# Optimization experiments

Measured on AMD Instinct MI355X. Metric: run time of the kernel, lower is better.

## Reference

```python
import jax, jax.numpy as jnp
import numpy as np
from jax import lax

P = 4
PSIZE = P * P
ITERS = 3
EPS = 1e-8
LAMBDA = 1e-3  # inverse-temperature used by the EM routing sigmoid (yl-1993 style)
LN2PI_HALF = 0.5 * float(np.log(2.0 * np.pi))


def extract_patches(x, K, stride, pad):
    """x: (b,h,w,c) -> (b,oh,ow,K*K,c) sliding-window patches."""
    if pad:
        x = jnp.pad(x, ((0, 0), (pad, pad), (pad, pad), (0, 0)))
    b, h, w, c = x.shape
    oh = (h - K) // stride + 1
    ow = (w - K) // stride + 1
    slices = []
    for ki in range(K):
        for kj in range(K):
            slices.append(x[:, ki:ki + stride * (oh - 1) + 1:stride,
                             kj:kj + stride * (ow - 1) + 1:stride, :])
    return jnp.stack(slices, axis=3)  # (b,oh,ow,K*K,c)


def em_routing(v, a_in, beta_u, beta_a, iters=ITERS):
    """EM routing (Hinton et al. 2018).
    v: (n, Bin, Cout, PSIZE) votes, a_in: (n, Bin, 1) input activations.
    Returns mu: (n, Cout, PSIZE), a_out: (n, Cout).
    """
    n, Bin, Cout, psize = v.shape
    r = jnp.full((n, Bin, Cout), 1.0 / Cout, dtype=v.dtype)
    mu = None
    a_out = None
    for it in range(iters):
        # ---- M step ----
        r_w = r * a_in                                    # (n,Bin,Cout)
        r_sum = r_w.sum(axis=1, keepdims=True)            # (n,1,Cout)
        coeff = (r_w / (r_sum + EPS))[..., None]          # (n,Bin,Cout,1)
        mu = jnp.sum(coeff * v, axis=1, keepdims=True)    # (n,1,Cout,psize)
        sigma_sq = jnp.sum(coeff * (v - mu) ** 2, axis=1, keepdims=True) + EPS
        cost_h = (beta_u[None, None, :, None] + 0.5 * jnp.log(sigma_sq)) * r_sum[..., None]
        a_out = jax.nn.sigmoid(LAMBDA * (beta_a[None, None, :] - cost_h.sum(axis=3)))  # (n,1,Cout)
        # ---- E step ----
        if it < iters - 1:
            ln_p = -(v - mu) ** 2 / (2.0 * sigma_sq) - 0.5 * jnp.log(sigma_sq) - LN2PI_HALF
            ln_ap = ln_p.sum(axis=3) + jnp.log(EPS + a_out)  # (n,Bin,Cout)
            r = jax.nn.softmax(ln_ap, axis=2)
    return mu[:, 0], a_out[:, 0]


def depthwise_caps(pose, a, W, bu, ba, K, stride):
    """DepthWiseConvCaps: each capsule type routes its own KxK spatial patch to one
    output capsule of the same type. W: (K*K, B, P, P)."""
    b = pose.shape[0]
    Bc = a.shape[-1]
    pad = K // 2
    pp = extract_patches(pose, K, stride, pad)  # (b,oh,ow,KK,B*PSIZE)
    ap = extract_patches(a, K, stride, pad)     # (b,oh,ow,KK,B)
    oh, ow = pp.shape[1], pp.shape[2]
    pm = pp.reshape(b, oh, ow, K * K, Bc, P, P)
    v = jnp.einsum('bhwkcij,kcjl->bhwkcil', pm, W)            # (b,oh,ow,KK,B,P,P)
    v = v.transpose(0, 1, 2, 4, 3, 5, 6).reshape(b * oh * ow * Bc, K * K, 1, PSIZE)
    a_in = ap.transpose(0, 1, 2, 4, 3).reshape(b * oh * ow * Bc, K * K, 1)
    mu, a_out = em_routing(v, a_in, bu, ba)
    return mu.reshape(b, oh, ow, Bc * PSIZE), a_out.reshape(b, oh, ow, Bc)


def conv_caps_1x1(pose, a, W, bu, ba):
    """ConvCaps with K=1, stride=1: per-position routing Bin -> Cout. W: (Bin,Cout,P,P)."""
    b, h, w, _ = pose.shape
    Bc, Cc = W.shape[0], W.shape[1]
    pm = pose.reshape(b * h * w, Bc, P, P)
    v = jnp.einsum('nbij,bcjl->nbcil', pm, W).reshape(b * h * w, Bc, Cc, PSIZE)
    a_in = a.reshape(b * h * w, Bc)[..., None]
    mu, a_out = em_routing(v, a_in, bu, ba)
    return mu.reshape(b, h, w, Cc * PSIZE), a_out.reshape(b, h, w, Cc)


def class_caps(pose, a, W, bu, ba):
    """Class ConvCaps: w_shared across positions + coordinate addition. W: (D,E,P,P)."""
    b, h, w, _ = pose.shape
    D, E = W.shape[0], W.shape[1]
    pm = pose.reshape(b, h, w, D, P, P)
    v = jnp.einsum('bhwdij,dejl->bhwdeil', pm, W).reshape(b, h, w, D, E, PSIZE)
    # coordinate addition on the first two vote components
    coord = jnp.zeros((h, w, PSIZE), v.dtype)
    coord = coord.at[:, :, 0].add(jnp.arange(h, dtype=v.dtype)[:, None] / h)
    coord = coord.at[:, :, 1].add(jnp.arange(w, dtype=v.dtype)[None, :] / w)
    v = v + coord[None, :, :, None, None, :]
    v = v.reshape(b, h * w * D, E, PSIZE)
    a_in = a.reshape(b, h * w * D, 1)
    mu, a_out = em_routing(v, a_in, bu, ba)
    return mu, a_out  # (b,E,PSIZE), (b,E)


def _forward(x, conv1_w, conv1_b, prim_pose_w, prim_pose_b, prim_a_w, prim_a_b,
             dw1_w, dw1_bu, dw1_ba, cc1_w, cc1_bu, cc1_ba,
             dw2_w, dw2_bu, dw2_ba, cc2_w, cc2_bu, cc2_ba,
             cls_w, cls_bu, cls_ba):
    # conv stem: k5 s2 valid
    y = lax.conv_general_dilated(x, conv1_w, (2, 2), 'VALID',
                                 dimension_numbers=('NHWC', 'HWIO', 'NHWC'))
    y = jax.nn.relu(y + conv1_b)
    # primary caps: 1x1 convs for pose and activation
    pose = jnp.einsum('bhwc,cd->bhwd', y, prim_pose_w) + prim_pose_b   # (b,h,w,B*PSIZE)
    a = jax.nn.sigmoid(jnp.einsum('bhwc,cd->bhwd', y, prim_a_w) + prim_a_b)  # (b,h,w,B)
    pose, a = depthwise_caps(pose, a, dw1_w, dw1_bu, dw1_ba, K=7, stride=2)
    pose, a = conv_caps_1x1(pose, a, cc1_w, cc1_bu, cc1_ba)
    pose, a = depthwise_caps(pose, a, dw2_w, dw2_bu, dw2_ba, K=5, stride=2)
    pose, a = conv_caps_1x1(pose, a, cc2_w, cc2_bu, cc2_ba)
    pose_cls, a_cls = class_caps(pose, a, cls_w, cls_bu, cls_ba)
    return a_cls  # (b, E)


def setup_inputs() -> dict:
    key = jax.random.key(0)
    ks = jax.random.split(key, 10)
    f32 = jnp.float32
    d = {}
    d['x'] = jax.random.normal(ks[0], (32, 64, 64, 1), f32)
    d['conv1_w'] = jax.random.normal(ks[1], (5, 5, 1, 64), f32) * 0.1
    d['conv1_b'] = jnp.zeros((64,), f32)
    d['prim_pose_w'] = jax.random.normal(ks[2], (64, 128), f32) * 0.1
    d['prim_pose_b'] = jnp.zeros((128,), f32)
    d['prim_a_w'] = jax.random.normal(ks[3], (64, 8), f32) * 0.1
    d['prim_a_b'] = jnp.zeros((8,), f32)
    d['dw1_w'] = jax.random.normal(ks[4], (49, 8, 4, 4), f32) * 0.25
    d['dw1_bu'] = jnp.zeros((1,), f32)
    d['dw1_ba'] = jnp.zeros((1,), f32)
    d['cc1_w'] = jax.random.normal(ks[5], (8, 16, 4, 4), f32) * 0.25
    d['cc1_bu'] = jnp.zeros((16,), f32)
    d['cc1_ba'] = jnp.zeros((16,), f32)
    d['dw2_w'] = jax.random.normal(ks[6], (25, 16, 4, 4), f32) * 0.25
    d['dw2_bu'] = jnp.zeros((1,), f32)
    d['dw2_ba'] = jnp.zeros((1,), f32)
    d['cc2_w'] = jax.random.normal(ks[7], (16, 16, 4, 4), f32) * 0.25
    d['cc2_bu'] = jnp.zeros((16,), f32)
    d['cc2_ba'] = jnp.zeros((16,), f32)
    d['cls_w'] = jax.random.normal(ks[8], (16, 10, 4, 4), f32) * 0.25
    d['cls_bu'] = jnp.zeros((10,), f32)
    d['cls_ba'] = jnp.zeros((10,), f32)
    return d


def reference(x, conv1_w, conv1_b, prim_pose_w, prim_pose_b, prim_a_w, prim_a_b,
              dw1_w, dw1_bu, dw1_ba, cc1_w, cc1_bu, cc1_ba,
              dw2_w, dw2_bu, dw2_ba, cc2_w, cc2_bu, cc2_ba,
              cls_w, cls_bu, cls_ba):
    return _forward(x, conv1_w, conv1_b, prim_pose_w, prim_pose_b, prim_a_w, prim_a_b,
                    dw1_w, dw1_bu, dw1_ba, cc1_w, cc1_bu, cc1_ba,
                    dw2_w, dw2_bu, dw2_ba, cc2_w, cc2_bu, cc2_ba,
                    cls_w, cls_bu, cls_ba)
```

## Files before the change

### kernel.cpp

```cpp
#include <hip/hip_runtime.h>
#include <hip/hip_bf16.h>

#define EPS 1e-8f
#define LAMBDA 1e-3f
#define LN2PI_HALF 0.9189385332046727f

__device__ __forceinline__ float sigmoidf(float x) { return 1.f / (1.f + __expf(-x)); }

__global__ __launch_bounds__(256) void stem_primary_kernel(
    const float* __restrict__ x, const float* __restrict__ w,
    const float* __restrict__ bias,
    const float* __restrict__ wp, const float* __restrict__ bp,
    const float* __restrict__ wa, const float* __restrict__ ba,
    float* __restrict__ pose, float* __restrict__ a) {
  __shared__ __align__(16) float wc_s[25][64];
  __shared__ __align__(16) float wa_s[64][8];
  __shared__ __align__(16) float bias_s[64];
  __shared__ __align__(16) float bp_s[128];
  __shared__ float ba_s[8];
  __shared__ float xs[5][63];
  __shared__ __align__(16) float ys_u[2][15][68];

  int t = threadIdx.x;
  int oi = blockIdx.x % 30;
  int b  = blockIdx.x / 30;

  for (int q = t; q < 400;  q += 256) ((float4*)wc_s)[q] = ((const float4*)w)[q];
  for (int q = t; q < 128;  q += 256) ((float4*)wa_s)[q] = ((const float4*)wa)[q];
  if (t < 64) bias_s[t] = bias[t];
  if (t < 128) bp_s[t] = bp[t];
  if (t < 8) ba_s[t] = ba[t];
  for (int q = t; q < 315; q += 256) {
    int ki = q / 63, col = q % 63;
    xs[ki][col] = x[(b * 64 + 2 * oi + ki) * 64 + col];
  }
  __syncthreads();

  for (int q = t; q < 480; q += 256) {
    int pos = q >> 4, c4 = (q & 15) << 2;
    float4 s4 = *(const float4*)&bias_s[c4];
#pragma unroll
    for (int ki = 0; ki < 5; ++ki)
#pragma unroll
      for (int kj = 0; kj < 5; ++kj) {
        float xv = xs[ki][2 * pos + kj];
        const float4 wv = *(const float4*)&wc_s[ki * 5 + kj][c4];
        s4.x += xv * wv.x;
        s4.y += xv * wv.y;
        s4.z += xv * wv.z;
        s4.w += xv * wv.w;
      }
    s4.x = fmaxf(s4.x, 0.f);
    s4.y = fmaxf(s4.y, 0.f);
    s4.z = fmaxf(s4.z, 0.f);
    s4.w = fmaxf(s4.w, 0.f);
    *(float4*)&ys_u[pos & 1][pos >> 1][c4] = s4;
  }
  __syncthreads();

  int w_ = t >> 7, d = t & 127;
  float acc[15];
#pragma unroll
  for (int j = 0; j < 15; ++j) acc[j] = bp_s[d];
  const float* wpd = wp + d;
#pragma unroll 4
  for (int c4 = 0; c4 < 64; c4 += 4) {
    float w0 = wpd[(c4 + 0) * 128];
    float w1 = wpd[(c4 + 1) * 128];
    float w2 = wpd[(c4 + 2) * 128];
    float w3 = wpd[(c4 + 3) * 128];
#pragma unroll
    for (int j = 0; j < 15; ++j) {
      const float4 yv = *(const float4*)&ys_u[w_][j][c4];
      acc[j] += yv.x * w0 + yv.y * w1 + yv.z * w2 + yv.w * w3;
    }
  }
  size_t rowb = (size_t)(b * 30 + oi) * 30;
#pragma unroll
  for (int j = 0; j < 15; ++j)
    pose[(rowb + w_ + 2 * j) * 128 + d] = acc[j];

  if (t < 240) {
    int pos = t >> 3, jj = t & 7;
    float s = ba_s[jj];
#pragma unroll 8
    for (int c = 0; c < 64; ++c) s += ys_u[pos & 1][pos >> 1][c] * wa_s[c][jj];
    a[(rowb + pos) * 8 + jj] = sigmoidf(s);
  }
}

template <int K, int BC, int HIN, int WIN, int HOUT, int WOUT, int OIG, int NG>
__global__ __launch_bounds__(256) void dw_caps_kernel(
    const float* __restrict__ pose_in, const float* __restrict__ a_in,
    const float* __restrict__ Wt,
    const float* __restrict__ bu_p, const float* __restrict__ ba_p,
    float* __restrict__ pose_out, float* __restrict__ a_out) {
  constexpr int PAD = K / 2;
  constexpr int RA = (2 * (OIG - 1) + K < HIN) ? (2 * (OIG - 1) + K) : HIN;
  constexpr int TOT = OIG * WOUT * 16;
  constexpr int KM = (TOT + 255) / 256;
  __shared__ __align__(16) float tp[RA * WIN * 20];
  __shared__ float ta[RA * WIN];
  __shared__ __align__(16) float wt[K * K * 16];

  int t = threadIdx.x;
  int g = (NG > 1) ? (blockIdx.x % NG) : 0;
  int c = (blockIdx.x / NG) % BC;
  int b = blockIdx.x / (NG * BC);
  int oi_lo = g * OIG;
  int rlo = max(0, 2 * oi_lo - PAD);
  int rhi = min(HIN, 2 * (oi_lo + OIG - 1) - PAD + K);
  int nrows = rhi - rlo;

  for (int q = t; q < K * K * 16; q += 256) {
    int tap = q >> 4, lj = q & 15, l = lj >> 2, j = lj & 3;
    wt[tap * 16 + lj] = Wt[((size_t)tap * BC + c) * 16 + j * 4 + l];
  }
  for (int q = t; q < nrows * WIN; q += 256) {
    int row = q / WIN, col = q % WIN;
    ta[q] = a_in[((size_t)((b * HIN + rlo + row) * WIN + col)) * BC + c];
  }
  for (int q = t; q < nrows * WIN * 4; q += 256) {
    int quad = q & 3, pc = q >> 2;
    int row = pc / WIN, col = pc % WIN;
    const float4 src = *(const float4*)(pose_in +
        (((size_t)((b * HIN + rlo + row) * WIN + col)) * BC + c) * 16 + quad * 4);
    *(float4*)(tp + (row * WIN + col) * 20 + quad * 4) = src;
  }
  __syncthreads();

  const int p = t & 15;
  const int ip = p >> 2, l = p & 3;
  const float* wtl = wt + l * 4;

  int ih0[KM], iw0[KM];
  float rsum[KM], acc[KM], acc2[KM];
#pragma unroll
  for (int k = 0; k < KM; ++k) {
    int s = t + k * 256;
    int pr = s >> 4;
    int oj = pr % WOUT;
    int oi = oi_lo + pr / WOUT;
    ih0[k] = 2 * oi - PAD;
    iw0[k] = 2 * oj - PAD;
    rsum[k] = 0.f;
    acc[k] = 0.f;
    acc2[k] = 0.f;
  }

#pragma unroll 1
  for (int ki = 0; ki < K; ++ki) {
    int rb[KM];
    bool vk[KM];
#pragma unroll
    for (int k = 0; k < KM; ++k) {
      int ih = ih0[k] + ki;
      vk[k] = (t + k * 256 < TOT) && (ih >= 0) && (ih < HIN);
      rb[k] = (ih - rlo) * WIN;
    }
#pragma unroll
    for (int kj = 0; kj < K; ++kj) {
      const float4 wr = *(const float4*)(wtl + (ki * K + kj) * 16);
#pragma unroll
      for (int k = 0; k < KM; ++k) {
        if (!vk[k]) continue;
        int iw = iw0[k] + kj;
        if (iw < 0 || iw >= WIN) continue;
        int idx = rb[k] + iw;
        float ak = ta[idx];
        const float4 pm = *(const float4*)(tp + idx * 20 + ip * 4);
        float v = pm.x * wr.x + pm.y * wr.y + pm.z * wr.z + pm.w * wr.w;
        rsum[k] += ak;
        float av = ak * v;
        acc[k] += av;
        acc2[k] += av * v;
      }
    }
  }

#pragma unroll 1
  for (int k = 0; k < KM; ++k) {
    int s = t + k * 256;
    if (s >= TOT) break;
    int pr = s >> 4;
    int oj = pr % WOUT;
    int oi = oi_lo + pr / WOUT;
    float inv = 1.f / (rsum[k] + EPS);
    float mu = acc[k] * inv;
    float S = rsum[k] * inv;
    float sg = acc2[k] * inv - mu * mu * (2.f - S);
    sg = fmaxf(sg, 0.f) + EPS;
    float hl = 0.5f * __logf(sg);
    float ls = hl;
    ls += __shfl_xor(ls, 1, 64);
    ls += __shfl_xor(ls, 2, 64);
    ls += __shfl_xor(ls, 4, 64);
    ls += __shfl_xor(ls, 8, 64);

    size_t obase = ((size_t)(b * HOUT + oi) * WOUT + oj) * BC + c;
    pose_out[obase * 16 + p] = mu;
    if (p == 0) {
      float cost = rsum[k] * (16.f * bu_p[0] + ls);
      a_out[obase] = sigmoidf(LAMBDA * (ba_p[0] - cost));
    }
  }
}

__global__ __launch_bounds__(256) void cc_em_coop8_kernel(
    const float* __restrict__ pose_in, const float* __restrict__ a_arr,
    const float* __restrict__ Wt,
    const float* __restrict__ bu_p, const float* __restrict__ ba_p,
    float* __restrict__ pose_out, float* __restrict__ a_out) {
  __shared__ float red_s[2][2][2][64 * 9];
  int t = threadIdx.x;
  int w = t >> 6, lane = t & 63;
  int prob = w >> 1, wh = w & 1;
  int c = lane >> 2, q = lane & 3;
  int n = blockIdx.x * 2 + prob;

  float ain[4], rw[4], v[4][4];
  const float* pbase = pose_in + (size_t)n * 128;
#pragma unroll
  for (int i = 0; i < 4; ++i) {
    int b = wh * 4 + i;
    ain[i] = a_arr[(size_t)n * 8 + b];
    rw[i] = (1.f / 16.f) * ain[i];
    const float4 pm = *(const float4*)(pbase + b * 16 + q * 4);
    const float* wr = Wt + (b * 16 + c) * 16;
    const float4 r0 = *(const float4*)(wr + 0);
    const float4 r1 = *(const float4*)(wr + 4);
    const float4 r2 = *(const float4*)(wr + 8);
    const float4 r3 = *(const float4*)(wr + 12);
    v[i][0] = pm.x * r0.x + pm.y * r1.x + pm.z * r2.x + pm.w * r3.x;
    v[i][1] = pm.x * r0.y + pm.y * r1.y + pm.z * r2.y + pm.w * r3.y;
    v[i][2] = pm.x * r0.z + pm.y * r1.z + pm.z * r2.z + pm.w * r3.z;
    v[i][3] = pm.x * r0.w + pm.y * r1.w + pm.z * r2.w + pm.w * r3.w;
  }
  float bu = bu_p[c], ba = ba_p[c];

  float mu[4], inv2[4], lsum = 0.f, ao = 0.f;
#pragma unroll 1
  for (int it = 0; it < 3; ++it) {
    float psA = 0.f, psV[4] = {0, 0, 0, 0}, psV2[4] = {0, 0, 0, 0};
#pragma unroll
    for (int i = 0; i < 4; ++i) {
      psA += rw[i];
#pragma unroll
      for (int l = 0; l < 4; ++l) {
        float rv = rw[i] * v[i][l];
        psV[l] += rv;
        psV2[l] += rv * v[i][l];
      }
    }
    {
      float* rs = &red_s[it & 1][prob][wh][lane * 9];
      rs[0] = psA;
#pragma unroll
      for (int l = 0; l < 4; ++l) { rs[1 + l] = psV[l]; rs[5 + l] = psV2[l]; }
    }
    __syncthreads();
    float sA = 0.f, sV[4] = {0, 0, 0, 0}, sV2[4] = {0, 0, 0, 0};
#pragma unroll
    for (int w2 = 0; w2 < 2; ++w2) {
      const float* rr = &red_s[it & 1][prob][w2][lane * 9];
      sA += rr[0];
#pragma unroll
      for (int l = 0; l < 4; ++l) { sV[l] += rr[1 + l]; sV2[l] += rr[5 + l]; }
    }
    float inv = 1.f / (sA + EPS);
    float S = sA * inv;
    lsum = 0.f;
#pragma unroll
    for (int l = 0; l < 4; ++l) {
      mu[l] = sV[l] * inv;
      float sg = sV2[l] * inv - mu[l] * mu[l] * (2.f - S) + EPS;
      sg = fmaxf(sg, EPS);
      inv2[l] = 0.5f / sg;
      lsum += 0.5f * __logf(sg);
    }
    lsum += __shfl_xor(lsum, 1, 64);
    lsum += __shfl_xor(lsum, 2, 64);
    float cost = sA * (16.f * bu + lsum);
    ao = sigmoidf(LAMBDA * (ba - cost));

    if (it < 2) {
      float term[4];
#pragma unroll
      for (int i = 0; i < 4; ++i) {
        float s = 0.f;
#pragma unroll
        for (int l = 0; l < 4; ++l) {
          float d = v[i][l] - mu[l];
          s += d * d * inv2[l];
        }
        term[i] = s;
      }
#pragma unroll
      for (int i = 0; i < 4; ++i) {
        term[i] += __shfl_xor(term[i], 1, 64);
        term[i] += __shfl_xor(term[i], 2, 64);
      }
      float basec = __logf(EPS + ao) - lsum - 16.f * LN2PI_HALF;
      float lnap[4], mx[4], Z[4];
#pragma unroll
      for (int i = 0; i < 4; ++i) { lnap[i] = basec - term[i]; mx[i] = lnap[i]; }
#pragma unroll
      for (int m = 4; m < 64; m <<= 1)
#pragma unroll
        for (int i = 0; i < 4; ++i) mx[i] = fmaxf(mx[i], __shfl_xor(mx[i], m, 64));
#pragma unroll
      for (int i = 0; i < 4; ++i) { lnap[i] = __expf(lnap[i] - mx[i]); Z[i] = lnap[i]; }
#pragma unroll
      for (int m = 4; m < 64; m <<= 1)
#pragma unroll
        for (int i = 0; i < 4; ++i) Z[i] += __shfl_xor(Z[i], m, 64);
#pragma unroll
      for (int i = 0; i < 4; ++i) rw[i] = lnap[i] / Z[i] * ain[i];
    }
  }
  if (wh == 0) {
    *(float4*)(pose_out + (size_t)n * 256 + c * 16 + q * 4) =
        make_float4(mu[0], mu[1], mu[2], mu[3]);
    if (q == 0) a_out[(size_t)n * 16 + c] = ao;
  }
}

__global__ __launch_bounds__(256) void cc_em_coop16_kernel(
    const float* __restrict__ pose_in, const float* __restrict__ a_arr,
    const float* __restrict__ Wt,
    const float* __restrict__ bu_p, const float* __restrict__ ba_p,
    float* __restrict__ pose_out, float* __restrict__ a_out) {
  __shared__ float red_s[2][4][64 * 9];
  int t = threadIdx.x;
  int w = t >> 6, lane = t & 63;
  int c = lane >> 2, q = lane & 3;
  int n = blockIdx.x;

  float ain[4], rw[4], v[4][4];
  const float* pbase = pose_in + (size_t)n * 256;
#pragma unroll
  for (int i = 0; i < 4; ++i) {
    int b = w * 4 + i;
    ain[i] = a_arr[(size_t)n * 16 + b];
    rw[i] = (1.f / 16.f) * ain[i];
    const float4 pm = *(const float4*)(pbase + b * 16 + q * 4);
    const float* wr = Wt + (b * 16 + c) * 16;
    const float4 r0 = *(const float4*)(wr + 0);
    const float4 r1 = *(const float4*)(wr + 4);
    const float4 r2 = *(const float4*)(wr + 8);
    const float4 r3 = *(const float4*)(wr + 12);
    v[i][0] = pm.x * r0.x + pm.y * r1.x + pm.z * r2.x + pm.w * r3.x;
    v[i][1] = pm.x * r0.y + pm.y * r1.y + pm.z * r2.y + pm.w * r3.y;
    v[i][2] = pm.x * r0.z + pm.y * r1.z + pm.z * r2.z + pm.w * r3.z;
    v[i][3] = pm.x * r0.w + pm.y * r1.w + pm.z * r2.w + pm.w * r3.w;
  }
  float bu = bu_p[c], ba = ba_p[c];

  float mu[4], inv2[4], lsum = 0.f, ao = 0.f;
#pragma unroll 1
  for (int it = 0; it < 3; ++it) {
    float psA = 0.f, psV[4] = {0, 0, 0, 0}, psV2[4] = {0, 0, 0, 0};
#pragma unroll
    for (int i = 0; i < 4; ++i) {
      psA += rw[i];
#pragma unroll
      for (int l = 0; l < 4; ++l) {
        float rv = rw[i] * v[i][l];
        psV[l] += rv;
        psV2[l] += rv * v[i][l];
      }
    }
    {
      float* rs = &red_s[it & 1][w][lane * 9];
      rs[0] = psA;
#pragma unroll
      for (int l = 0; l < 4; ++l) { rs[1 + l] = psV[l]; rs[5 + l] = psV2[l]; }
    }
    __syncthreads();
    float sA = 0.f, sV[4] = {0, 0, 0, 0}, sV2[4] = {0, 0, 0, 0};
#pragma unroll
    for (int w2 = 0; w2 < 4; ++w2) {
      const float* rr = &red_s[it & 1][w2][lane * 9];
      sA += rr[0];
#pragma unroll
      for (int l = 0; l < 4; ++l) { sV[l] += rr[1 + l]; sV2[l] += rr[5 + l]; }
    }
    float inv = 1.f / (sA + EPS);
    float S = sA * inv;
    lsum = 0.f;
#pragma unroll
    for (int l = 0; l < 4; ++l) {
      mu[l] = sV[l] * inv;
      float sg = sV2[l] * inv - mu[l] * mu[l] * (2.f - S) + EPS;
      sg = fmaxf(sg, EPS);
      inv2[l] = 0.5f / sg;
      lsum += 0.5f * __logf(sg);
    }
    lsum += __shfl_xor(lsum, 1, 64);
    lsum += __shfl_xor(lsum, 2, 64);
    float cost = sA * (16.f * bu + lsum);
    ao = sigmoidf(LAMBDA * (ba - cost));

    if (it < 2) {
      float term[4];
#pragma unroll
      for (int i = 0; i < 4; ++i) {
        float s = 0.f;
#pragma unroll
        for (int l = 0; l < 4; ++l) {
          float d = v[i][l] - mu[l];
          s += d * d * inv2[l];
        }
        term[i] = s;
      }
#pragma unroll
      for (int i = 0; i < 4; ++i) {
        term[i] += __shfl_xor(term[i], 1, 64);
        term[i] += __shfl_xor(term[i], 2, 64);
      }
      float basec = __logf(EPS + ao) - lsum - 16.f * LN2PI_HALF;
      float lnap[4], mx[4], Z[4];
#pragma unroll
      for (int i = 0; i < 4; ++i) { lnap[i] = basec - term[i]; mx[i] = lnap[i]; }
#pragma unroll
      for (int m = 4; m < 64; m <<= 1)
#pragma unroll
        for (int i = 0; i < 4; ++i) mx[i] = fmaxf(mx[i], __shfl_xor(mx[i], m, 64));
#pragma unroll
      for (int i = 0; i < 4; ++i) { lnap[i] = __expf(lnap[i] - mx[i]); Z[i] = lnap[i]; }
#pragma unroll
      for (int m = 4; m < 64; m <<= 1)
#pragma unroll
        for (int i = 0; i < 4; ++i) Z[i] += __shfl_xor(Z[i], m, 64);
#pragma unroll
      for (int i = 0; i < 4; ++i) rw[i] = lnap[i] / Z[i] * ain[i];
    }
  }
  if (w == 0) {
    *(float4*)(pose_out + (size_t)n * 256 + c * 16 + q * 4) =
        make_float4(mu[0], mu[1], mu[2], mu[3]);
    if (q == 0) a_out[(size_t)n * 16 + c] = ao;
  }
}

__global__ __launch_bounds__(256) void cls_m_kernel(
    const float* __restrict__ pose5, const float* __restrict__ a5,
    const float* __restrict__ X, const float* __restrict__ W,
    const float* __restrict__ bu_p, const float* __restrict__ ba_p,
    float* __restrict__ mu_g, float* __restrict__ inv2_g,
    float* __restrict__ base_g, float* __restrict__ out,
    int first, int last) {
  int blk = blockIdx.x;
  int c = blk % 10, b = blk / 10;
  int t = threadIdx.x;
  int lane = t & 63, wv = t >> 6;
  const float* pg = pose5 + (size_t)b * 16384;
  __shared__ float w_s[16][16];
  {
    int d = t & 15, jj = t >> 4;
    w_s[jj][d] = W[(d * 10 + c) * 16 + jj];
  }
  __syncthreads();
  const int d = t & 15;
  float wf[16];
#pragma unroll
  for (int jj = 0; jj < 16; ++jj) wf[jj] = w_s[jj][d];

  float sA = 0.f, sV[16], sV2[16];
#pragma unroll
  for (int p = 0; p < 16; ++p) { sV[p] = 0.f; sV2[p] = 0.f; }
#pragma unroll 1
  for (int rep = 0; rep < 4; ++rep) {
    int bi = rep * 256 + t;
    int pos = bi >> 4;
    float rw = first ? 0.1f * a5[(size_t)b * 1024 + bi]
                     : X[(size_t)blk * 1024 + bi];
    float ci = (float)(pos >> 3) * 0.125f;
    float cj = (float)(pos & 7) * 0.125f;
    const float* pp = pg + pos * 256 + d * 16;
    float pmr[16];
#pragma unroll
    for (int q = 0; q < 16; ++q) pmr[q] = pp[q];
    sA += rw;
#pragma unroll
    for (int p = 0; p < 16; ++p) {
      int ip = p >> 2, l = p & 3;
      float v = pmr[ip * 4 + 0] * wf[0 * 4 + l] + pmr[ip * 4 + 1] * wf[1 * 4 + l]
              + pmr[ip * 4 + 2] * wf[2 * 4 + l] + pmr[ip * 4 + 3] * wf[3 * 4 + l];
      if (p == 0) v += ci;
      else if (p == 1) v += cj;
      float rv = rw * v;
      sV[p] += rv;
      sV2[p] += rv * v;
    }
  }
#pragma unroll
  for (int off = 1; off < 64; off <<= 1) {
    sA += __shfl_xor(sA, off, 64);
#pragma unroll
    for (int p = 0; p < 16; ++p) {
      sV[p]  += __shfl_xor(sV[p],  off, 64);
      sV2[p] += __shfl_xor(sV2[p], off, 64);
    }
  }
  __shared__ float red[4][36];
  if (lane == 0) {
    red[wv][0] = sA;
#pragma unroll
    for (int p = 0; p < 16; ++p) { red[wv][1 + p] = sV[p]; red[wv][17 + p] = sV2[p]; }
  }
  __syncthreads();
  if (t < 16) {
    int p = t;
    float sAf  = red[0][0] + red[1][0] + red[2][0] + red[3][0];
    float sVf  = red[0][1+p] + red[1][1+p] + red[2][1+p] + red[3][1+p];
    float sV2f = red[0][17+p] + red[1][17+p] + red[2][17+p] + red[3][17+p];
    float inv = 1.f / (sAf + EPS);
    float S = sAf * inv;
    float mu = sVf * inv;
    float sg = sV2f * inv - mu * mu * (2.f - S) + EPS;
    sg = fmaxf(sg, EPS);
    mu_g[blk * 16 + p] = mu;
    inv2_g[blk * 16 + p] = 0.5f / sg;
    float hl = 0.5f * __logf(sg);
    float lsum = hl;
    lsum += __shfl_xor(lsum, 1, 64);
    lsum += __shfl_xor(lsum, 2, 64);
    lsum += __shfl_xor(lsum, 4, 64);
    lsum += __shfl_xor(lsum, 8, 64);
    if (p == 0) {
      float cost = sAf * (16.f * bu_p[c] + lsum);
      float ao = sigmoidf(LAMBDA * (ba_p[c] - cost));
      base_g[blk] = __logf(EPS + ao) - lsum - 16.f * LN2PI_HALF;
      if (last) out[blk] = ao;
    }
  }
}

__global__ __launch_bounds__(256) void cls_e_kernel(
    const float* __restrict__ pose5, const float* __restrict__ a5,
    const float* __restrict__ W,
    const float* __restrict__ mu_g, const float* __restrict__ inv2_g,
    const float* __restrict__ base_g, float* __restrict__ X) {
  int b = blockIdx.x >> 2;
  int t = threadIdx.x;
  int bi = ((blockIdx.x & 3) << 8) + t;
  const float* pg = pose5 + (size_t)b * 16384;
  __shared__ float w2[10][16][16];
  __shared__ float mu_s[160];
  __shared__ float inv2_s[160];
  __shared__ float base_s[10];
  for (int q = t; q < 2560; q += 256) {
    int dd = q & 15, jj = (q >> 4) & 15, c = q >> 8;
    w2[c][jj][dd] = W[(dd * 10 + c) * 16 + jj];
  }
  if (t < 160) { mu_s[t] = mu_g[b * 160 + t]; inv2_s[t] = inv2_g[b * 160 + t]; }
  if (t >= 160 && t < 170) base_s[t - 160] = base_g[b * 10 + (t - 160)];
  __syncthreads();

  int pos = bi >> 4, d2 = bi & 15;
  float ci = (float)(pos >> 3) * 0.125f;
  float cj = (float)(pos & 7) * 0.125f;
  const float* pp = pg + pos * 256 + d2 * 16;
  float pmr[16];
#pragma unroll
  for (int q = 0; q < 16; ++q) pmr[q] = pp[q];
  float lnap[10];
#pragma unroll 1
  for (int c = 0; c < 10; ++c) {
    float wf[16];
#pragma unroll
    for (int jj = 0; jj < 16; ++jj) wf[jj] = w2[c][jj][d2];
    float s = base_s[c];
#pragma unroll
    for (int p = 0; p < 16; ++p) {
      int ip = p >> 2, l = p & 3;
      float v = pmr[ip * 4 + 0] * wf[0 * 4 + l] + pmr[ip * 4 + 1] * wf[1 * 4 + l]
              + pmr[ip * 4 + 2] * wf[2 * 4 + l] + pmr[ip * 4 + 3] * wf[3 * 4 + l];
      if (p == 0) v += ci;
      else if (p == 1) v += cj;
      float dd = v - mu_s[c * 16 + p];
      s -= dd * dd * inv2_s[c * 16 + p];
    }
    lnap[c] = s;
  }
  float m = -1e30f;
#pragma unroll
  for (int c = 0; c < 10; ++c) m = fmaxf(m, lnap[c]);
  float Z = 0.f;
  float ex[10];
#pragma unroll
  for (int c = 0; c < 10; ++c) { ex[c] = __expf(lnap[c] - m); Z += ex[c]; }
  float invZ = a5[(size_t)b * 1024 + bi] / Z;
#pragma unroll
  for (int c = 0; c < 10; ++c) X[((size_t)(b * 10 + c)) * 1024 + bi] = ex[c] * invZ;
}

extern "C" void kernel_launch(void* const* d_in, const int* in_sizes, int n_in,
                              void* d_out, int out_size, void* d_ws, size_t ws_size,
                              hipStream_t stream) {
  const float* x       = (const float*)d_in[0];
  const float* conv1_w = (const float*)d_in[1];
  const float* conv1_b = (const float*)d_in[2];
  const float* pp_w    = (const float*)d_in[3];
  const float* pp_b    = (const float*)d_in[4];
  const float* pa_w    = (const float*)d_in[5];
  const float* pa_b    = (const float*)d_in[6];
  const float* dw1_w   = (const float*)d_in[7];
  const float* dw1_bu  = (const float*)d_in[8];
  const float* dw1_ba  = (const float*)d_in[9];
  const float* cc1_w   = (const float*)d_in[10];
  const float* cc1_bu  = (const float*)d_in[11];
  const float* cc1_ba  = (const float*)d_in[12];
  const float* dw2_w   = (const float*)d_in[13];
  const float* dw2_bu  = (const float*)d_in[14];
  const float* dw2_ba  = (const float*)d_in[15];
  const float* cc2_w   = (const float*)d_in[16];
  const float* cc2_bu  = (const float*)d_in[17];
  const float* cc2_ba  = (const float*)d_in[18];
  const float* cls_w   = (const float*)d_in[19];
  const float* cls_bu  = (const float*)d_in[20];
  const float* cls_ba  = (const float*)d_in[21];
  float* out = (float*)d_out;

  float* ws = (float*)d_ws;
  float* pose1 = ws;
  float* a1    = ws + 3686400;
  float* pose2 = ws + 3916800;
  float* a2    = ws + 4838400;
  float* pose3 = ws;
  float* a3    = ws + 1843200;
  float* pose4 = ws + 1958400;
  float* a4    = ws + 2482688;
  float* pose5 = ws + 2515456;
  float* a5    = ws + 3039744;
  float* Xbuf  = ws + 3072512;
  float* mu_g  = ws + 3400192;
  float* inv2_g= ws + 3405312;
  float* base_g= ws + 3410432;

  stem_primary_kernel<<<960, 256, 0, stream>>>(x, conv1_w, conv1_b,
                                               pp_w, pp_b, pa_w, pa_b, pose1, a1);
  dw_caps_kernel<7, 8, 30, 30, 15, 15, 3, 5><<<1280, 256, 0, stream>>>(
      pose1, a1, dw1_w, dw1_bu, dw1_ba, pose2, a2);
  cc_em_coop8_kernel<<<3600, 256, 0, stream>>>(pose2, a2, cc1_w, cc1_bu, cc1_ba,
                                               pose3, a3);
  dw_caps_kernel<5, 16, 15, 15, 8, 8, 2, 4><<<2048, 256, 0, stream>>>(
      pose3, a3, dw2_w, dw2_bu, dw2_ba, pose4, a4);
  cc_em_coop16_kernel<<<2048, 256, 0, stream>>>(pose4, a4, cc2_w, cc2_bu, cc2_ba,
                                                pose5, a5);
  cls_m_kernel<<<320, 256, 0, stream>>>(pose5, a5, Xbuf, cls_w, cls_bu, cls_ba,
                                        mu_g, inv2_g, base_g, out, 1, 0);
  cls_e_kernel<<<128, 256, 0, stream>>>(pose5, a5, cls_w, mu_g, inv2_g, base_g, Xbuf);
  cls_m_kernel<<<320, 256, 0, stream>>>(pose5, a5, Xbuf, cls_w, cls_bu, cls_ba,
                                        mu_g, inv2_g, base_g, out, 0, 0);
  cls_e_kernel<<<128, 256, 0, stream>>>(pose5, a5, cls_w, mu_g, inv2_g, base_g, Xbuf);
  cls_m_kernel<<<320, 256, 0, stream>>>(pose5, a5, Xbuf, cls_w, cls_bu, cls_ba,
                                        mu_g, inv2_g, base_g, out, 0, 1);
}
```

Baseline: 250.3 us.

## Fuse class-capsule E-step into M-step kernel with ping-pong routing buffers

Merges the class-layer E step into the following M step, so each (batch, class) block recomputes the softmax over all 10 classes for its own inputs instead of reading a precomputed responsibility buffer. This drops two launches and the global round-trip through the X buffer. In exchange every block redoes the vote and log-likelihood computation for all classes, roughly ten times the E-step arithmetic. Double-buffered mu/inv2/base arrays prevent read/write races between iterations.

```diff
diff --git a/kernel.cpp b/kernel.cpp
--- a/kernel.cpp
+++ b/kernel.cpp
@@ -445,11 +445,10 @@
 
 __global__ __launch_bounds__(256) void cls_m_kernel(
     const float* __restrict__ pose5, const float* __restrict__ a5,
-    const float* __restrict__ X, const float* __restrict__ W,
+    const float* __restrict__ W,
     const float* __restrict__ bu_p, const float* __restrict__ ba_p,
     float* __restrict__ mu_g, float* __restrict__ inv2_g,
-    float* __restrict__ base_g, float* __restrict__ out,
-    int first, int last) {
+    float* __restrict__ base_g) {
   int blk = blockIdx.x;
   int c = blk % 10, b = blk / 10;
   int t = threadIdx.x;
@@ -473,8 +472,7 @@
   for (int rep = 0; rep < 4; ++rep) {
     int bi = rep * 256 + t;
     int pos = bi >> 4;
-    float rw = first ? 0.1f * a5[(size_t)b * 1024 + bi]
-                     : X[(size_t)blk * 1024 + bi];
+    float rw = 0.1f * a5[(size_t)b * 1024 + bi];
     float ci = (float)(pos >> 3) * 0.125f;
     float cj = (float)(pos & 7) * 0.125f;
     const float* pp = pg + pos * 256 + d * 16;
@@ -532,68 +530,129 @@
       float cost = sAf * (16.f * bu_p[c] + lsum);
       float ao = sigmoidf(LAMBDA * (ba_p[c] - cost));
       base_g[blk] = __logf(EPS + ao) - lsum - 16.f * LN2PI_HALF;
-      if (last) out[blk] = ao;
     }
   }
 }
 
-__global__ __launch_bounds__(256) void cls_e_kernel(
+__global__ __launch_bounds__(256) void cls_em_kernel(
     const float* __restrict__ pose5, const float* __restrict__ a5,
     const float* __restrict__ W,
-    const float* __restrict__ mu_g, const float* __restrict__ inv2_g,
-    const float* __restrict__ base_g, float* __restrict__ X) {
-  int b = blockIdx.x >> 2;
+    const float* __restrict__ bu_p, const float* __restrict__ ba_p,
+    const float* __restrict__ mu_in, const float* __restrict__ inv2_in,
+    const float* __restrict__ base_in,
+    float* __restrict__ mu_o, float* __restrict__ inv2_o,
+    float* __restrict__ base_o, float* __restrict__ out, int last) {
+  int blk = blockIdx.x;
+  int c_m = blk % 10, b = blk / 10;
   int t = threadIdx.x;
-  int bi = ((blockIdx.x & 3) << 8) + t;
+  int lane = t & 63, wv = t >> 6;
   const float* pg = pose5 + (size_t)b * 16384;
+
   __shared__ float w2[10][16][16];
   __shared__ float mu_s[160];
   __shared__ float inv2_s[160];
   __shared__ float base_s[10];
+  __shared__ float red[4][36];
+
   for (int q = t; q < 2560; q += 256) {
     int dd = q & 15, jj = (q >> 4) & 15, c = q >> 8;
     w2[c][jj][dd] = W[(dd * 10 + c) * 16 + jj];
   }
-  if (t < 160) { mu_s[t] = mu_g[b * 160 + t]; inv2_s[t] = inv2_g[b * 160 + t]; }
-  if (t >= 160 && t < 170) base_s[t - 160] = base_g[b * 10 + (t - 160)];
+  if (t < 160) { mu_s[t] = mu_in[b * 160 + t]; inv2_s[t] = inv2_in[b * 160 + t]; }
+  if (t >= 160 && t < 170) base_s[t - 160] = base_in[b * 10 + (t - 160)];
   __syncthreads();
 
-  int pos = bi >> 4, d2 = bi & 15;
-  float ci = (float)(pos >> 3) * 0.125f;
-  float cj = (float)(pos & 7) * 0.125f;
-  const float* pp = pg + pos * 256 + d2 * 16;
-  float pmr[16];
-#pragma unroll
-  for (int q = 0; q < 16; ++q) pmr[q] = pp[q];
-  float lnap[10];
+  const int d = t & 15;
+  float sA = 0.f, sV[16], sV2[16];
+#pragma unroll
+  for (int p = 0; p < 16; ++p) { sV[p] = 0.f; sV2[p] = 0.f; }
+
 #pragma unroll 1
-  for (int c = 0; c < 10; ++c) {
-    float wf[16];
-#pragma unroll
-    for (int jj = 0; jj < 16; ++jj) wf[jj] = w2[c][jj][d2];
-    float s = base_s[c];
+  for (int rep = 0; rep < 4; ++rep) {
+    int bi = rep * 256 + t;
+    int pos = bi >> 4;
+    float ci = (float)(pos >> 3) * 0.125f;
+    float cj = (float)(pos & 7) * 0.125f;
+    const float* pp = pg + pos * 256 + d * 16;
+    float pmr[16];
+#pragma unroll
+    for (int q = 0; q < 16; ++q) pmr[q] = pp[q];
+    float ain = a5[(size_t)b * 1024 + bi];
+
+    float vc[16];
+    float m_r = -1e30f, Z_r = 0.f, lnap_cm = 0.f;
+#pragma unroll 1
+    for (int c = 0; c < 10; ++c) {
+      float wf[16];
+#pragma unroll
+      for (int jj = 0; jj < 16; ++jj) wf[jj] = w2[c][jj][d];
+      float s = base_s[c];
+#pragma unroll
+      for (int p = 0; p < 16; ++p) {
+        int ip = p >> 2, l = p & 3;
+        float v = pmr[ip * 4 + 0] * wf[0 * 4 + l] + pmr[ip * 4 + 1] * wf[1 * 4 + l]
+                + pmr[ip * 4 + 2] * wf[2 * 4 + l] + pmr[ip * 4 + 3] * wf[3 * 4 + l];
+        if (p == 0) v += ci;
+        else if (p == 1) v += cj;
+        if (c == c_m) vc[p] = v;
+        float dd2 = v - mu_s[c * 16 + p];
+        s -= dd2 * dd2 * inv2_s[c * 16 + p];
+      }
+      if (c == c_m) lnap_cm = s;
+      if (s > m_r) { Z_r = Z_r * __expf(m_r - s) + 1.f; m_r = s; }
+      else Z_r += __expf(s - m_r);
+    }
+    float rw = __expf(lnap_cm - m_r) / Z_r * ain;
+
+    sA += rw;
 #pragma unroll
     for (int p = 0; p < 16; ++p) {
-      int ip = p >> 2, l = p & 3;
-      float v = pmr[ip * 4 + 0] * wf[0 * 4 + l] + pmr[ip * 4 + 1] * wf[1 * 4 + l]
-              + pmr[ip * 4 + 2] * wf[2 * 4 + l] + pmr[ip * 4 + 3] * wf[3 * 4 + l];
-      if (p == 0) v += ci;
-      else if (p == 1) v += cj;
-      float dd = v - mu_s[c * 16 + p];
-      s -= dd * dd * inv2_s[c * 16 + p];
-    }
-    lnap[c] = s;
-  }
-  float m = -1e30f;
-#pragma unroll
-  for (int c = 0; c < 10; ++c) m = fmaxf(m, lnap[c]);
-  float Z = 0.f;
-  float ex[10];
-#pragma unroll
-  for (int c = 0; c < 10; ++c) { ex[c] = __expf(lnap[c] - m); Z += ex[c]; }
-  float invZ = a5[(size_t)b * 1024 + bi] / Z;
-#pragma unroll
-  for (int c = 0; c < 10; ++c) X[((size_t)(b * 10 + c)) * 1024 + bi] = ex[c] * invZ;
+      float rv = rw * vc[p];
+      sV[p] += rv;
+      sV2[p] += rv * vc[p];
+    }
+  }
+
+#pragma unroll
+  for (int off = 1; off < 64; off <<= 1) {
+    sA += __shfl_xor(sA, off, 64);
+#pragma unroll
+    for (int p = 0; p < 16; ++p) {
+      sV[p]  += __shfl_xor(sV[p],  off, 64);
+      sV2[p] += __shfl_xor(sV2[p], off, 64);
+    }
+  }
+  if (lane == 0) {
+    red[wv][0] = sA;
+#pragma unroll
+    for (int p = 0; p < 16; ++p) { red[wv][1 + p] = sV[p]; red[wv][17 + p] = sV2[p]; }
+  }
+  __syncthreads();
+  if (t < 16) {
+    int p = t;
+    float sAf  = red[0][0] + red[1][0] + red[2][0] + red[3][0];
+    float sVf  = red[0][1+p] + red[1][1+p] + red[2][1+p] + red[3][1+p];
+    float sV2f = red[0][17+p] + red[1][17+p] + red[2][17+p] + red[3][17+p];
+    float inv = 1.f / (sAf + EPS);
+    float S = sAf * inv;
+    float mu = sVf * inv;
+    float sg = sV2f * inv - mu * mu * (2.f - S) + EPS;
+    sg = fmaxf(sg, EPS);
+    mu_o[blk * 16 + p] = mu;
+    inv2_o[blk * 16 + p] = 0.5f / sg;
+    float hl = 0.5f * __logf(sg);
+    float lsum = hl;
+    lsum += __shfl_xor(lsum, 1, 64);
+    lsum += __shfl_xor(lsum, 2, 64);
+    lsum += __shfl_xor(lsum, 4, 64);
+    lsum += __shfl_xor(lsum, 8, 64);
+    if (p == 0) {
+      float cost = sAf * (16.f * bu_p[c_m] + lsum);
+      float ao = sigmoidf(LAMBDA * (ba_p[c_m] - cost));
+      base_o[blk] = __logf(EPS + ao) - lsum - 16.f * LN2PI_HALF;
+      if (last) out[blk] = ao;
+    }
+  }
 }
 
 extern "C" void kernel_launch(void* const* d_in, const int* in_sizes, int n_in,
@@ -634,10 +693,12 @@
   float* a4    = ws + 2482688;
   float* pose5 = ws + 2515456;
   float* a5    = ws + 3039744;
-  float* Xbuf  = ws + 3072512;
-  float* mu_g  = ws + 3400192;
-  float* inv2_g= ws + 3405312;
-  float* base_g= ws + 3410432;
+  float* mu_gA  = ws + 3072512;
+  float* inv2_gA= ws + 3077632;
+  float* base_gA= ws + 3082752;
+  float* mu_gB  = ws + 3083072;
+  float* inv2_gB= ws + 3088192;
+  float* base_gB= ws + 3093312;
 
   stem_primary_kernel<<<960, 256, 0, stream>>>(x, conv1_w, conv1_b,
                                                pp_w, pp_b, pa_w, pa_b, pose1, a1);
@@ -649,12 +710,12 @@
       pose3, a3, dw2_w, dw2_bu, dw2_ba, pose4, a4);
   cc_em_coop16_kernel<<<2048, 256, 0, stream>>>(pose4, a4, cc2_w, cc2_bu, cc2_ba,
                                                 pose5, a5);
-  cls_m_kernel<<<320, 256, 0, stream>>>(pose5, a5, Xbuf, cls_w, cls_bu, cls_ba,
-                                        mu_g, inv2_g, base_g, out, 1, 0);
-  cls_e_kernel<<<128, 256, 0, stream>>>(pose5, a5, cls_w, mu_g, inv2_g, base_g, Xbuf);
-  cls_m_kernel<<<320, 256, 0, stream>>>(pose5, a5, Xbuf, cls_w, cls_bu, cls_ba,
-                                        mu_g, inv2_g, base_g, out, 0, 0);
-  cls_e_kernel<<<128, 256, 0, stream>>>(pose5, a5, cls_w, mu_g, inv2_g, base_g, Xbuf);
-  cls_m_kernel<<<320, 256, 0, stream>>>(pose5, a5, Xbuf, cls_w, cls_bu, cls_ba,
-                                        mu_g, inv2_g, base_g, out, 0, 1);
+  cls_m_kernel<<<320, 256, 0, stream>>>(pose5, a5, cls_w, cls_bu, cls_ba,
+                                        mu_gA, inv2_gA, base_gA);
+  cls_em_kernel<<<320, 256, 0, stream>>>(pose5, a5, cls_w, cls_bu, cls_ba,
+                                         mu_gA, inv2_gA, base_gA,
+                                         mu_gB, inv2_gB, base_gB, out, 0);
+  cls_em_kernel<<<320, 256, 0, stream>>>(pose5, a5, cls_w, cls_bu, cls_ba,
+                                         mu_gB, inv2_gB, base_gB,
+                                         mu_gA, inv2_gA, base_gA, out, 1);
 }
```

New measurement: 306.2 us. 1.22x slower.
